# Performance work log

Hardware: AMD Instinct MI355X
Metric: run time of the kernel (lower is better)

The kernel has to match this reference:

```python
import jax, jax.numpy as jnp
import numpy as np

EPS = 1e-8  # torch F.cosine_similarity default eps


def setup_inputs() -> dict:
    key = jax.random.key(0)
    k1, k2 = jax.random.split(key)
    x = jax.random.normal(k1, (16384, 1024), dtype=jnp.float32)
    label = jax.random.randint(k2, (16384, 64), 0, 2).astype(jnp.int64)
    w = jnp.asarray(10.0, dtype=jnp.float32)  # nn.Parameter init_w
    b = jnp.asarray(-5.0, dtype=jnp.float32)  # nn.Parameter init_b
    return {"x": x, "label": label, "w": w, "b": b}


def reference(x, label, w, b):
    # Append the 'no-label' column for rows whose label vector is all zero.
    extra = (label.sum(axis=1) == 0).astype(label.dtype)[:, None]
    lab = jnp.concatenate([label, extra], axis=1).astype(x.dtype)  # [B, C]

    counts = lab.sum(axis=0)                  # [C] positives per centroid
    active = counts > 0                       # torch drops empty columns; we mask them

    # Centroids: mean of x over rows carrying each label (scatter-mean as GEMM).
    anchor = (lab.T @ x) / jnp.maximum(counts, 1.0)[:, None]   # [C, D]

    # Cosine similarity between every sample and every centroid.
    xn = jnp.maximum(jnp.linalg.norm(x, axis=1), EPS)          # [B]
    an = jnp.maximum(jnp.linalg.norm(anchor, axis=1), EPS)     # [C]
    cos = (x @ anchor.T) / (xn[:, None] * an[None, :])          # [B, C]

    logits = cos * w + b
    # Removing empty columns from softmax == setting their logits to -inf.
    logits = jnp.where(active[None, :], logits, -jnp.inf)
    logp = jax.nn.log_softmax(logits, axis=1)                   # [B, C]

    # Row expansion in torch duplicates sample i once per positive label j;
    # the logits row only depends on i, so CE over expanded rows is a
    # pair-weighted mean of -logp[i, j] over positive (i, j) pairs.
    n_pairs = lab.sum()
    nloss = -jnp.sum(jnp.where(lab > 0, logp, 0.0)) / n_pairs
    return nloss
```

## Files before the change

### kernel.cpp

```cpp
#include <hip/hip_runtime.h>
#include <hip/hip_bf16.h>
#include <stdint.h>

#define NROWS 16384
#define NDIM  1024
#define NLAB  64
#define NC    65
#define CPAD  80

typedef float float4v __attribute__((ext_vector_type(4)));
typedef short short8  __attribute__((ext_vector_type(8)));

static constexpr size_t SCALE_B = 0;
static constexpr size_t ACTB_B  = 320;
static constexpr size_t WSUM_B  = 400;
static constexpr size_t DONE_B  = 404;
static constexpr size_t CNTF_B  = 448;
static constexpr size_t CNTP_B  = 1024;
static constexpr size_t MASK_B  = 83968;
static constexpr size_t XN2_B   = 215040;
static constexpr size_t LFRAG_B = 280576;
static constexpr size_t BFRAG_B = 2902016;
static constexpr size_t XAF_B   = 3065856;
static constexpr size_t PART_B  = 36620288;
static constexpr size_t SLAB    = (size_t)CPAD * NDIM * 4;

__device__ __forceinline__ unsigned short bf16u(float f) {
    __hip_bfloat16 h = __float2bfloat16(f);
    return __builtin_bit_cast(unsigned short, h);
}
__device__ __forceinline__ unsigned pk2(float a, float b) {
    return (unsigned)bf16u(a) | ((unsigned)bf16u(b) << 16);
}

__global__ __launch_bounds__(256) void kP_prep(const float* __restrict__ x,
                                               const int* __restrict__ label,
                                               unsigned short* __restrict__ xAfrag,
                                               float* __restrict__ xn2g,
                                               unsigned long long* __restrict__ masks,
                                               unsigned* __restrict__ cntpart,
                                               unsigned short* __restrict__ lfrag) {
    __shared__ float red2[4][16];
    __shared__ unsigned cnt[NC];
    __shared__ unsigned long long smask[64];
    int t = threadIdx.x;
    int wave = t >> 6, lane = t & 63;
    int q = lane >> 4, col = lane & 15;
    if (blockIdx.x < 1024) {
        int rt = blockIdx.x;
        const float* rowp = x + ((size_t)rt * 16 + col) * NDIM;
        uint4* dst = (uint4*)xAfrag + ((size_t)rt * 32 + wave * 8) * 64 + lane;
        float4 fa[8], fb[8];
#pragma unroll
        for (int kb = 0; kb < 8; ++kb) {
            int d0 = wave * 256 + kb * 32 + q * 8;
            fa[kb] = *(const float4*)(rowp + d0);
            fb[kb] = *(const float4*)(rowp + d0 + 4);
        }
        float sq = 0.f;
#pragma unroll
        for (int kb = 0; kb < 8; ++kb) {
            sq += fa[kb].x * fa[kb].x + fa[kb].y * fa[kb].y + fa[kb].z * fa[kb].z + fa[kb].w * fa[kb].w
                + fb[kb].x * fb[kb].x + fb[kb].y * fb[kb].y + fb[kb].z * fb[kb].z + fb[kb].w * fb[kb].w;
            uint4 v;
            v.x = pk2(fa[kb].x, fa[kb].y); v.y = pk2(fa[kb].z, fa[kb].w);
            v.z = pk2(fb[kb].x, fb[kb].y); v.w = pk2(fb[kb].z, fb[kb].w);
            dst[kb * 64] = v;
        }
        sq += __shfl_xor(sq, 16, 64);
        sq += __shfl_xor(sq, 32, 64);
        if (q == 0) red2[wave][col] = sq;
        __syncthreads();
        if (t < 16) xn2g[rt * 16 + t] = red2[0][t] + red2[1][t] + red2[2][t] + red2[3][t];
        return;
    }
    int bid = blockIdx.x - 1024;
    if (t < NC) cnt[t] = 0;
    __syncthreads();
    int rowblock = bid * 64;
    unsigned creg = 0, zreg = 0;
#pragma unroll 4
    for (int p = 0; p < 16; ++p) {
        int row = rowblock + p * 4 + wave;
        int v = label[row * NLAB + lane];
        unsigned long long m = __ballot(v != 0);
        creg += (unsigned)((m >> lane) & 1ull);
        if (lane == 0) {
            masks[row] = m;
            smask[p * 4 + wave] = m;
            zreg += (m == 0ull) ? 1u : 0u;
        }
    }
    atomicAdd(&cnt[lane], creg);
    if (lane == 0 && zreg) atomicAdd(&cnt[64], zreg);
    __syncthreads();
    if (t < 80) cntpart[bid * 80 + t] = (t < NC) ? cnt[t] : 0u;
    for (int pid = t; pid < 640; pid += 256) {
        int rt2l = pid / 320, rem = pid % 320;
        int ct = rem >> 6, ln = rem & 63;
        int qq = ln >> 4, cc = ln & 15;
        int c = ct * 16 + cc;
        int rbase = rt2l * 32 + qq * 8;
        unsigned pk[4];
#pragma unroll
        for (int jp = 0; jp < 4; ++jp) {
            unsigned long long m0 = smask[rbase + jp * 2], m1 = smask[rbase + jp * 2 + 1];
            unsigned b0, b1;
            if (c < 64)       { b0 = (unsigned)((m0 >> c) & 1ull); b1 = (unsigned)((m1 >> c) & 1ull); }
            else if (c == 64) { b0 = (m0 == 0ull); b1 = (m1 == 0ull); }
            else              { b0 = 0u; b1 = 0u; }
            pk[jp] = (b0 ? 0x3F80u : 0u) | (b1 ? 0x3F800000u : 0u);
        }
        uint4 w = make_uint4(pk[0], pk[1], pk[2], pk[3]);
        ((uint4*)lfrag)[((size_t)(bid * 2 + rt2l) * 5 + ct) * 64 + ln] = w;
    }
}

__global__ __launch_bounds__(256) void kB_sums(const float* __restrict__ x,
                                               const unsigned short* __restrict__ lfrag,
                                               float* __restrict__ partial,
                                               int kslices) {
    __shared__ float xt[2][32][65];
    int t = threadIdx.x, wave = t >> 6, lane = t & 63;
    int q = lane >> 4, col = lane & 15;
    int dgroup = blockIdx.x & 15, ks = blockIdx.x >> 4;
    int nkb = (NROWS / kslices) >> 5;
    int kb0 = ks * nkb;
    int d = dgroup * 64 + wave * 16 + col;
    const uint4* A = (const uint4*)lfrag;
    int srow = t >> 3, sd = (t & 7) * 8;

    float4v acc[5];
#pragma unroll
    for (int ct = 0; ct < 5; ++ct) acc[ct] = (float4v){0.f, 0.f, 0.f, 0.f};

    {
        const float* g = x + ((size_t)(kb0 * 32 + srow)) * NDIM + dgroup * 64 + sd;
        float4 u = *(const float4*)g, v2 = *(const float4*)(g + 4);
        float* L = &xt[0][srow][sd];
        L[0] = u.x; L[1] = u.y; L[2] = u.z; L[3] = u.w;
        L[4] = v2.x; L[5] = v2.y; L[6] = v2.z; L[7] = v2.w;
    }
    __syncthreads();

    for (int i = 0; i < nkb; ++i) {
        int cur = i & 1;
        float4 u, v2;
        bool havenext = (i + 1) < nkb;
        if (havenext) {
            const float* g = x + ((size_t)((kb0 + i + 1) * 32 + srow)) * NDIM + dgroup * 64 + sd;
            u = *(const float4*)g; v2 = *(const float4*)(g + 4);
        }
        int kb = kb0 + i;
        uint4 a0[5];
#pragma unroll
        for (int ct = 0; ct < 5; ++ct) a0[ct] = A[((size_t)kb * 5 + ct) * 64 + lane];
        float f[8];
#pragma unroll
        for (int j = 0; j < 8; ++j) f[j] = xt[cur][q * 8 + j][wave * 16 + col];
        uint4 bq;
        bq.x = pk2(f[0], f[1]); bq.y = pk2(f[2], f[3]);
        bq.z = pk2(f[4], f[5]); bq.w = pk2(f[6], f[7]);
        short8 bf = __builtin_bit_cast(short8, bq);
#pragma unroll
        for (int ct = 0; ct < 5; ++ct) {
            short8 af = __builtin_bit_cast(short8, a0[ct]);
            acc[ct] = __builtin_amdgcn_mfma_f32_16x16x32_bf16(af, bf, acc[ct], 0, 0, 0);
        }
        if (havenext) {
            float* L = &xt[cur ^ 1][srow][sd];
            L[0] = u.x; L[1] = u.y; L[2] = u.z; L[3] = u.w;
            L[4] = v2.x; L[5] = v2.y; L[6] = v2.z; L[7] = v2.w;
        }
        __syncthreads();
    }
    float* pb = partial + (size_t)ks * CPAD * NDIM;
#pragma unroll
    for (int ct = 0; ct < 5; ++ct)
#pragma unroll
        for (int reg = 0; reg < 4; ++reg)
            pb[(size_t)(ct * 16 + q * 4 + reg) * NDIM + d] = acc[ct][reg];
}

__global__ __launch_bounds__(1024) void kC_fuse(const float* __restrict__ wptr,
                                                const unsigned* __restrict__ cntpart,
                                                const float* __restrict__ partial,
                                                int kslices,
                                                unsigned short* __restrict__ bfrag,
                                                float* __restrict__ scale,
                                                unsigned char* __restrict__ actB,
                                                unsigned* __restrict__ countsF,
                                                float* __restrict__ wsum,
                                                unsigned* __restrict__ done) {
    int c = blockIdx.x, t = threadIdx.x;
    __shared__ float red[16];
    __shared__ unsigned credu[4];
    __shared__ float bcast[1];
    if (c == 0 && t == 512) *wsum = 0.f;
    if (c == 0 && t == 513) *done = 0u;
    if (t < 256) {
        unsigned cv = cntpart[t * 80 + c];
#pragma unroll
        for (int m = 32; m >= 1; m >>= 1) cv += __shfl_xor(cv, m, 64);
        if ((t & 63) == 0) credu[t >> 6] = cv;
    }
    const float* p = partial + (size_t)c * NDIM + t;
    float s = 0.f;
#pragma unroll 8
    for (int sl = 0; sl < kslices; ++sl) s += p[(size_t)sl * CPAD * NDIM];
    float ss = s * s;
#pragma unroll
    for (int m = 32; m >= 1; m >>= 1) ss += __shfl_xor(ss, m, 64);
    if ((t & 63) == 0) red[t >> 6] = ss;
    __syncthreads();
    if (t == 0) {
        float tot = 0.f;
#pragma unroll
        for (int j = 0; j < 16; ++j) tot += red[j];
        bcast[0] = sqrtf(tot);
    }
    unsigned cnt = credu[0] + credu[1] + credu[2] + credu[3];
    __syncthreads();
    float invc = 1.0f / (float)(cnt > 0u ? cnt : 1u);
    float a = s * invc;
    float an = fmaxf(bcast[0] * invc, 1e-8f);
    unsigned short h = bf16u(a / an);
    int ct = c >> 4, colc = c & 15;
    int kb = t >> 5, q = (t >> 3) & 3, j0 = t & 7;
    bfrag[((((size_t)ct * 32 + kb) * 64) + q * 16 + colc) * 8 + j0] = h;
    float hv = __bfloat162float(__builtin_bit_cast(__hip_bfloat16, h));
    float nb2 = hv * hv;
#pragma unroll
    for (int m = 32; m >= 1; m >>= 1) nb2 += __shfl_xor(nb2, m, 64);
    if ((t & 63) == 0) red[t >> 6] = nb2;
    __syncthreads();
    if (t == 0) {
        float n2 = 0.f;
#pragma unroll
        for (int j = 0; j < 16; ++j) n2 += red[j];
        scale[c] = (n2 > 0.f) ? (wptr[0] / sqrtf(n2)) : 0.f;
        actB[c] = (cnt > 0u) ? 1 : 0;
        countsF[c] = cnt;
    }
}

__global__ __launch_bounds__(256) void k3_loss(const unsigned short* __restrict__ xAfrag,
                                               const unsigned short* __restrict__ bfrag,
                                               const float* __restrict__ xn2g,
                                               const unsigned long long* __restrict__ masks,
                                               const unsigned char* __restrict__ actB,
                                               const float* __restrict__ scale,
                                               const float* __restrict__ bptr,
                                               float* __restrict__ wsum,
                                               unsigned* __restrict__ done,
                                               const unsigned* __restrict__ countsF,
                                               float* __restrict__ out) {
    __shared__ float redsm[3][64][21];
    int t = threadIdx.x, wave = t >> 6, lane = t & 63;
    int q = lane >> 4, col = lane & 15;
    int rt = blockIdx.x;
    int rowbase = rt * 16;
    const uint4* A = (const uint4*)xAfrag + (size_t)rt * 32 * 64 + lane;
    const uint4* Bp = (const uint4*)bfrag + lane;
    int kb0 = wave * 8;

    float4v acc[5];
#pragma unroll
    for (int ct = 0; ct < 5; ++ct) acc[ct] = (float4v){0.f, 0.f, 0.f, 0.f};

    uint4 a0 = A[(size_t)(kb0 + 0) * 64], a1 = A[(size_t)(kb0 + 1) * 64];
    uint4 b0[5], b1[5];
#pragma unroll
    for (int ct = 0; ct < 5; ++ct) b0[ct] = Bp[(size_t)(ct * 32 + kb0 + 0) * 64];
#pragma unroll
    for (int ct = 0; ct < 5; ++ct) b1[ct] = Bp[(size_t)(ct * 32 + kb0 + 1) * 64];

    for (int s = 0; s < 8; s += 2) {
        int p2 = s + 2 < 8 ? kb0 + s + 2 : kb0 + s;
        int p3 = s + 3 < 8 ? kb0 + s + 3 : kb0 + s + 1;
        {
            short8 af = __builtin_bit_cast(short8, a0);
#pragma unroll
            for (int ct = 0; ct < 5; ++ct) {
                short8 bf = __builtin_bit_cast(short8, b0[ct]);
                acc[ct] = __builtin_amdgcn_mfma_f32_16x16x32_bf16(af, bf, acc[ct], 0, 0, 0);
            }
            a0 = A[(size_t)p2 * 64];
#pragma unroll
            for (int ct = 0; ct < 5; ++ct) b0[ct] = Bp[(size_t)(ct * 32 + p2) * 64];
        }
        {
            short8 af = __builtin_bit_cast(short8, a1);
#pragma unroll
            for (int ct = 0; ct < 5; ++ct) {
                short8 bf = __builtin_bit_cast(short8, b1[ct]);
                acc[ct] = __builtin_amdgcn_mfma_f32_16x16x32_bf16(af, bf, acc[ct], 0, 0, 0);
            }
            a1 = A[(size_t)p3 * 64];
#pragma unroll
            for (int ct = 0; ct < 5; ++ct) b1[ct] = Bp[(size_t)(ct * 32 + p3) * 64];
        }
    }

    if (wave) {
#pragma unroll
        for (int ct = 0; ct < 5; ++ct)
#pragma unroll
            for (int reg = 0; reg < 4; ++reg)
                redsm[wave - 1][lane][ct * 4 + reg] = acc[ct][reg];
    }
    __syncthreads();
    if (wave != 0) return;
#pragma unroll
    for (int w = 0; w < 3; ++w)
#pragma unroll
        for (int ct = 0; ct < 5; ++ct)
#pragma unroll
            for (int reg = 0; reg < 4; ++reg)
                acc[ct][reg] += redsm[w][lane][ct * 4 + reg];

    float bv = bptr[0];
    float sc[5]; unsigned char ab[5];
#pragma unroll
    for (int ct = 0; ct < 5; ++ct) { sc[ct] = scale[ct * 16 + col]; ab[ct] = actB[ct * 16 + col]; }

    float contrib = 0.f;
#pragma unroll
    for (int reg = 0; reg < 4; ++reg) {
        int rl = q * 4 + reg;
        int row = rowbase + rl;
        float inv = 1.0f / fmaxf(sqrtf(xn2g[row]), 1e-8f);
        unsigned long long mask = masks[row];
        float v[5]; float lmax = -1e30f;
#pragma unroll
        for (int ct = 0; ct < 5; ++ct) {
            float lg = acc[ct][reg] * sc[ct] * inv + bv;
            v[ct] = ab[ct] ? lg : -1e30f;
            lmax = fmaxf(lmax, v[ct]);
        }
#pragma unroll
        for (int m = 1; m < 16; m <<= 1) lmax = fmaxf(lmax, __shfl_xor(lmax, m, 16));
        float es = 0.f;
#pragma unroll
        for (int ct = 0; ct < 5; ++ct) es += expf(v[ct] - lmax);
#pragma unroll
        for (int m = 1; m < 16; m <<= 1) es += __shfl_xor(es, m, 16);
        float lse = lmax + logf(es);
        float ps = 0.f;
#pragma unroll
        for (int ct = 0; ct < 5; ++ct) {
            int c = ct * 16 + col;
            bool pos = (c < 64) ? (((mask >> c) & 1ull) != 0ull)
                                : ((c == 64) ? (mask == 0ull) : false);
            ps += pos ? v[ct] : 0.f;
        }
#pragma unroll
        for (int m = 1; m < 16; m <<= 1) ps += __shfl_xor(ps, m, 16);
        float npos = mask ? (float)__popcll(mask) : 1.0f;
        float crow = ps - npos * lse;
        if (col == 0) contrib += crow;
    }
#pragma unroll
    for (int m = 1; m < 64; m <<= 1) contrib += __shfl_xor(contrib, m, 64);
    if (lane == 0) {
        atomicAdd(wsum, contrib);
        __threadfence();
        unsigned prev = atomicAdd(done, 1u);
        if (prev == (unsigned)gridDim.x - 1u) {
            __threadfence();
            float wv = __hip_atomic_load(wsum, __ATOMIC_ACQUIRE, __HIP_MEMORY_SCOPE_AGENT);
            float np = 0.f;
            for (int c = 0; c < NC; ++c) np += (float)countsF[c];
            out[0] = -wv / np;
        }
    }
}

extern "C" void kernel_launch(void* const* d_in, const int* in_sizes, int n_in,
                              void* d_out, int out_size, void* d_ws, size_t ws_size,
                              hipStream_t stream) {
    (void)in_sizes; (void)n_in; (void)out_size;
    const float* x = (const float*)d_in[0];
    const int* label = (const int*)d_in[1];
    const float* w = (const float*)d_in[2];
    const float* b = (const float*)d_in[3];

    char* ws = (char*)d_ws;
    float* scale = (float*)(ws + SCALE_B);
    unsigned char* actB = (unsigned char*)(ws + ACTB_B);
    float* wsum = (float*)(ws + WSUM_B);
    unsigned* done = (unsigned*)(ws + DONE_B);
    unsigned* countsF = (unsigned*)(ws + CNTF_B);
    unsigned* cntpart = (unsigned*)(ws + CNTP_B);
    unsigned long long* masks = (unsigned long long*)(ws + MASK_B);
    float* xn2g = (float*)(ws + XN2_B);
    unsigned short* lfrag = (unsigned short*)(ws + LFRAG_B);
    unsigned short* bfrag = (unsigned short*)(ws + BFRAG_B);
    unsigned short* xAfrag = (unsigned short*)(ws + XAF_B);
    float* partial = (float*)(ws + PART_B);

    int kslices = 64;
    while (kslices > 8 && PART_B + (size_t)kslices * SLAB > ws_size) kslices >>= 1;

    hipLaunchKernelGGL(kP_prep, dim3(1024 + 256), dim3(256), 0, stream,
                       x, label, xAfrag, xn2g, masks, cntpart, lfrag);
    hipLaunchKernelGGL(kB_sums, dim3(16 * kslices), dim3(256), 0, stream,
                       x, lfrag, partial, kslices);
    hipLaunchKernelGGL(kC_fuse, dim3(CPAD), dim3(1024), 0, stream,
                       w, cntpart, partial, kslices, bfrag, scale, actB, countsF, wsum, done);
    hipLaunchKernelGGL(k3_loss, dim3(NROWS / 16), dim3(256), 0, stream,
                       xAfrag, bfrag, xn2g, masks, actB, scale, b, wsum, done, countsF, (float*)d_out);
}
```

Before: 176.5 us.

## Move x bf16 packing into GEMM kernel, preload A fragments, relax fence

The x-to-bf16 fragment packing and row-norm blocks move out of the prep kernel and into the centroid-sum kernel's grid. The prep kernel now only processes labels, so its short launch no longer has to read all of x before the sums GEMM can start. The loss kernel now loads all eight A fragments up front instead of double-buffering them. The final-block handoff replaces __threadfence with a vmcnt wait, which may weaken memory ordering for the atomic reduction.

```diff
diff --git a/kernel.cpp b/kernel.cpp
--- a/kernel.cpp
+++ b/kernel.cpp
@@ -33,50 +33,17 @@
     return (unsigned)bf16u(a) | ((unsigned)bf16u(b) << 16);
 }
 
-__global__ __launch_bounds__(256) void kP_prep(const float* __restrict__ x,
-                                               const int* __restrict__ label,
-                                               unsigned short* __restrict__ xAfrag,
-                                               float* __restrict__ xn2g,
-                                               unsigned long long* __restrict__ masks,
-                                               unsigned* __restrict__ cntpart,
-                                               unsigned short* __restrict__ lfrag) {
-    __shared__ float red2[4][16];
+__global__ __launch_bounds__(256) void kA_labels(const int* __restrict__ label,
+                                                 unsigned long long* __restrict__ masks,
+                                                 unsigned* __restrict__ cntpart,
+                                                 unsigned short* __restrict__ lfrag) {
     __shared__ unsigned cnt[NC];
     __shared__ unsigned long long smask[64];
     int t = threadIdx.x;
+    int bid = blockIdx.x;
+    if (t < NC) cnt[t] = 0;
+    __syncthreads();
     int wave = t >> 6, lane = t & 63;
-    int q = lane >> 4, col = lane & 15;
-    if (blockIdx.x < 1024) {
-        int rt = blockIdx.x;
-        const float* rowp = x + ((size_t)rt * 16 + col) * NDIM;
-        uint4* dst = (uint4*)xAfrag + ((size_t)rt * 32 + wave * 8) * 64 + lane;
-        float4 fa[8], fb[8];
-#pragma unroll
-        for (int kb = 0; kb < 8; ++kb) {
-            int d0 = wave * 256 + kb * 32 + q * 8;
-            fa[kb] = *(const float4*)(rowp + d0);
-            fb[kb] = *(const float4*)(rowp + d0 + 4);
-        }
-        float sq = 0.f;
-#pragma unroll
-        for (int kb = 0; kb < 8; ++kb) {
-            sq += fa[kb].x * fa[kb].x + fa[kb].y * fa[kb].y + fa[kb].z * fa[kb].z + fa[kb].w * fa[kb].w
-                + fb[kb].x * fb[kb].x + fb[kb].y * fb[kb].y + fb[kb].z * fb[kb].z + fb[kb].w * fb[kb].w;
-            uint4 v;
-            v.x = pk2(fa[kb].x, fa[kb].y); v.y = pk2(fa[kb].z, fa[kb].w);
-            v.z = pk2(fb[kb].x, fb[kb].y); v.w = pk2(fb[kb].z, fb[kb].w);
-            dst[kb * 64] = v;
-        }
-        sq += __shfl_xor(sq, 16, 64);
-        sq += __shfl_xor(sq, 32, 64);
-        if (q == 0) red2[wave][col] = sq;
-        __syncthreads();
-        if (t < 16) xn2g[rt * 16 + t] = red2[0][t] + red2[1][t] + red2[2][t] + red2[3][t];
-        return;
-    }
-    int bid = blockIdx.x - 1024;
-    if (t < NC) cnt[t] = 0;
-    __syncthreads();
     int rowblock = bid * 64;
     unsigned creg = 0, zreg = 0;
 #pragma unroll 4
@@ -116,13 +83,47 @@
     }
 }
 
-__global__ __launch_bounds__(256) void kB_sums(const float* __restrict__ x,
-                                               const unsigned short* __restrict__ lfrag,
-                                               float* __restrict__ partial,
-                                               int kslices) {
+__global__ __launch_bounds__(256) void kBP(const float* __restrict__ x,
+                                           const unsigned short* __restrict__ lfrag,
+                                           float* __restrict__ partial,
+                                           unsigned short* __restrict__ xAfrag,
+                                           float* __restrict__ xn2g,
+                                           int kslices) {
     __shared__ float xt[2][32][65];
+    __shared__ float red2[4][16];
     int t = threadIdx.x, wave = t >> 6, lane = t & 63;
     int q = lane >> 4, col = lane & 15;
+    int ngemm = 16 * kslices;
+
+    if ((int)blockIdx.x >= ngemm) {
+        int rt = blockIdx.x - ngemm;
+        const float* rowp = x + ((size_t)rt * 16 + col) * NDIM;
+        uint4* dst = (uint4*)xAfrag + ((size_t)rt * 32 + wave * 8) * 64 + lane;
+        float4 fa[8], fb[8];
+#pragma unroll
+        for (int kb = 0; kb < 8; ++kb) {
+            int d0 = wave * 256 + kb * 32 + q * 8;
+            fa[kb] = *(const float4*)(rowp + d0);
+            fb[kb] = *(const float4*)(rowp + d0 + 4);
+        }
+        float sq = 0.f;
+#pragma unroll
+        for (int kb = 0; kb < 8; ++kb) {
+            sq += fa[kb].x * fa[kb].x + fa[kb].y * fa[kb].y + fa[kb].z * fa[kb].z + fa[kb].w * fa[kb].w
+                + fb[kb].x * fb[kb].x + fb[kb].y * fb[kb].y + fb[kb].z * fb[kb].z + fb[kb].w * fb[kb].w;
+            uint4 v;
+            v.x = pk2(fa[kb].x, fa[kb].y); v.y = pk2(fa[kb].z, fa[kb].w);
+            v.z = pk2(fb[kb].x, fb[kb].y); v.w = pk2(fb[kb].z, fb[kb].w);
+            dst[kb * 64] = v;
+        }
+        sq += __shfl_xor(sq, 16, 64);
+        sq += __shfl_xor(sq, 32, 64);
+        if (q == 0) red2[wave][col] = sq;
+        __syncthreads();
+        if (t < 16) xn2g[rt * 16 + t] = red2[0][t] + red2[1][t] + red2[2][t] + red2[3][t];
+        return;
+    }
+
     int dgroup = blockIdx.x & 15, ks = blockIdx.x >> 4;
     int nkb = (NROWS / kslices) >> 5;
     int kb0 = ks * nkb;
@@ -268,7 +269,9 @@
 #pragma unroll
     for (int ct = 0; ct < 5; ++ct) acc[ct] = (float4v){0.f, 0.f, 0.f, 0.f};
 
-    uint4 a0 = A[(size_t)(kb0 + 0) * 64], a1 = A[(size_t)(kb0 + 1) * 64];
+    uint4 a[8];
+#pragma unroll
+    for (int j = 0; j < 8; ++j) a[j] = A[(size_t)(kb0 + j) * 64];
     uint4 b0[5], b1[5];
 #pragma unroll
     for (int ct = 0; ct < 5; ++ct) b0[ct] = Bp[(size_t)(ct * 32 + kb0 + 0) * 64];
@@ -279,24 +282,22 @@
         int p2 = s + 2 < 8 ? kb0 + s + 2 : kb0 + s;
         int p3 = s + 3 < 8 ? kb0 + s + 3 : kb0 + s + 1;
         {
-            short8 af = __builtin_bit_cast(short8, a0);
+            short8 af = __builtin_bit_cast(short8, a[s]);
 #pragma unroll
             for (int ct = 0; ct < 5; ++ct) {
                 short8 bf = __builtin_bit_cast(short8, b0[ct]);
                 acc[ct] = __builtin_amdgcn_mfma_f32_16x16x32_bf16(af, bf, acc[ct], 0, 0, 0);
             }
-            a0 = A[(size_t)p2 * 64];
 #pragma unroll
             for (int ct = 0; ct < 5; ++ct) b0[ct] = Bp[(size_t)(ct * 32 + p2) * 64];
         }
         {
-            short8 af = __builtin_bit_cast(short8, a1);
+            short8 af = __builtin_bit_cast(short8, a[s + 1]);
 #pragma unroll
             for (int ct = 0; ct < 5; ++ct) {
                 short8 bf = __builtin_bit_cast(short8, b1[ct]);
                 acc[ct] = __builtin_amdgcn_mfma_f32_16x16x32_bf16(af, bf, acc[ct], 0, 0, 0);
             }
-            a1 = A[(size_t)p3 * 64];
 #pragma unroll
             for (int ct = 0; ct < 5; ++ct) b1[ct] = Bp[(size_t)(ct * 32 + p3) * 64];
         }
@@ -364,10 +365,9 @@
     for (int m = 1; m < 64; m <<= 1) contrib += __shfl_xor(contrib, m, 64);
     if (lane == 0) {
         atomicAdd(wsum, contrib);
-        __threadfence();
+        asm volatile("s_waitcnt vmcnt(0)" ::: "memory");
         unsigned prev = atomicAdd(done, 1u);
         if (prev == (unsigned)gridDim.x - 1u) {
-            __threadfence();
             float wv = __hip_atomic_load(wsum, __ATOMIC_ACQUIRE, __HIP_MEMORY_SCOPE_AGENT);
             float np = 0.f;
             for (int c = 0; c < NC; ++c) np += (float)countsF[c];
@@ -402,10 +402,10 @@
     int kslices = 64;
     while (kslices > 8 && PART_B + (size_t)kslices * SLAB > ws_size) kslices >>= 1;
 
-    hipLaunchKernelGGL(kP_prep, dim3(1024 + 256), dim3(256), 0, stream,
-                       x, label, xAfrag, xn2g, masks, cntpart, lfrag);
-    hipLaunchKernelGGL(kB_sums, dim3(16 * kslices), dim3(256), 0, stream,
-                       x, lfrag, partial, kslices);
+    hipLaunchKernelGGL(kA_labels, dim3(256), dim3(256), 0, stream,
+                       label, masks, cntpart, lfrag);
+    hipLaunchKernelGGL(kBP, dim3(16 * kslices + 1024), dim3(256), 0, stream,
+                       x, lfrag, partial, xAfrag, xn2g, kslices);
     hipLaunchKernelGGL(kC_fuse, dim3(CPAD), dim3(1024), 0, stream,
                        w, cntpart, partial, kslices, bfrag, scale, actB, countsF, wsum, done);
     hipLaunchKernelGGL(k3_loss, dim3(NROWS / 16), dim3(256), 0, stream,
```

Result: faster. 172.1 us (-2.5%).
